# Performance work log

Hardware: AMD Instinct MI355X
Metric: run time of the kernel (lower is better)

The kernel has to match this reference:

```python
import jax, jax.numpy as jnp
import numpy as np
import math

N_HEADS = 4
N_ITERS = 2  # SSFormer n=2; each loop iteration recomputes the same values (no feedback in the original code)
BN_EPS = 1e-5


def _attention(q, k, v):
    """SSTransformer: multi-head cross-attention over flattened spatial dims.
    q,k,v: [B, C, H, W] -> returns [B, C, L] with L = H*W.
    """
    b, c = q.shape[0], q.shape[1]
    L = q.shape[2] * q.shape[3]
    ch = c // N_HEADS
    scale = 1.0 / math.sqrt(math.sqrt(ch))
    qf = (q.reshape(b * N_HEADS, ch, L) * scale)
    kf = (k.reshape(b * N_HEADS, ch, L) * scale)
    vf = v.reshape(b * N_HEADS, ch, L)
    # weight: [B*H, t, s]
    w = jnp.einsum('bct,bcs->bts', qf, kf)
    w = jax.nn.softmax(w.astype(jnp.float32), axis=-1).astype(w.dtype)
    a = jnp.einsum('bts,bcs->bct', w, vf)
    return a.reshape(b, c, L)


def setup_inputs() -> dict:
    key = jax.random.key(0)
    k1, k2, k3, k4 = jax.random.split(key, 4)
    B, C, H, W = 8, 512, 32, 32
    c = jax.random.normal(k1, (B, C, H, W), dtype=jnp.float32)
    e = jax.random.normal(k2, (B, C, H, W), dtype=jnp.float32)
    conv_w = jax.random.normal(k3, (C, C, 1, 1), dtype=jnp.float32) / math.sqrt(C)
    conv_b = jax.random.normal(k4, (C,), dtype=jnp.float32) * 0.02
    bn_gamma = jnp.ones((C,), dtype=jnp.float32)
    bn_beta = jnp.zeros((C,), dtype=jnp.float32)
    return {"c": c, "e": e, "conv_w": conv_w, "conv_b": conv_b,
            "bn_gamma": bn_gamma, "bn_beta": bn_beta}


def reference(c, e, conv_w, conv_b, bn_gamma, bn_beta):
    bs, ch, h, w = c.shape
    L = h * w
    for _ in range(N_ITERS):
        _c = _attention(e, c, c)                       # [B, C, L]
        _e = _attention(_c.reshape(bs, ch, h, w), e, e)  # [B, C, L]
    _e = _e.reshape(bs, ch, h, w)
    # Proj: 1x1 conv + BatchNorm2d (training-mode batch stats) + Swish
    x = jnp.einsum('oc,bchw->bohw', conv_w.reshape(ch, ch), _e) + conv_b[None, :, None, None]
    mean = jnp.mean(x, axis=(0, 2, 3), keepdims=True)
    var = jnp.var(x, axis=(0, 2, 3), keepdims=True)
    xn = (x - mean) * jax.lax.rsqrt(var + BN_EPS)
    xn = xn * bn_gamma[None, :, None, None] + bn_beta[None, :, None, None]
    return xn * jax.nn.sigmoid(xn)
```

## Files before the change

### kernel.cpp

```cpp
#include <hip/hip_runtime.h>
#include <hip/hip_bf16.h>

typedef __attribute__((ext_vector_type(8))) short short8;
typedef __attribute__((ext_vector_type(4))) float floatx4;
typedef __attribute__((ext_vector_type(4))) float f32x4;
typedef unsigned short u16;
typedef unsigned int u32;
typedef __attribute__((ext_vector_type(2))) unsigned int u32x2;
typedef __attribute__((ext_vector_type(4))) unsigned int u32x4;
typedef __attribute__((ext_vector_type(8))) unsigned short ushort8;

#define LSEQ 1024
#define CHD  128
#define CEXP 0.12751744900425577f
#define THR_RAW 62.73318f

static __device__ __forceinline__ u16 f2b(float f) {
  __hip_bfloat16 h = __float2bfloat16(f);
  return *reinterpret_cast<u16*>(&h);
}
static __device__ __forceinline__ u32 cvtpk(float a, float b) {
  u32 r;
  asm("v_cvt_pk_bf16_f32 %0, %1, %2" : "=v"(r) : "v"(a), "v"(b));
  return r;
}
static __device__ __forceinline__ float exp2f_fast(float x) {
  float r;
  asm("v_exp_f32 %0, %1" : "=v"(r) : "v"(x));
  return r;
}
static __device__ __forceinline__ void gl_lds16(const void* g, void* l) {
  __builtin_amdgcn_global_load_lds((__attribute__((address_space(1))) const void*)g,
                                   (__attribute__((address_space(3))) void*)l, 16, 0, 0);
}

__global__ __launch_bounds__(256) void k_prep(const float* __restrict__ cin,
                                              const float* __restrict__ ein,
                                              const float* __restrict__ Wf,
                                              u16* __restrict__ cV, u16* __restrict__ cT,
                                              u16* __restrict__ eV, u16* __restrict__ eT,
                                              u16* __restrict__ wb, float* __restrict__ zbuf) {
  __shared__ u16 tile[32][72];
  int z = blockIdx.z;
  int tid = threadIdx.x;
  if (z >= 64) {
    int wblk = (z - 64) * 64 + blockIdx.y * 16 + blockIdx.x;
    int base = (wblk * 256 + tid) * 8;
    f32x4 a = *(const f32x4*)(Wf + base);
    f32x4 b = *(const f32x4*)(Wf + base + 4);
    u32x4 u;
    u[0] = cvtpk(a[0], a[1]); u[1] = cvtpk(a[2], a[3]);
    u[2] = cvtpk(b[0], b[1]); u[3] = cvtpk(b[2], b[3]);
    *(u32x4*)(wb + base) = u;
    if (wblk == 0) {
      f32x4 zz; zz[0]=0.f; zz[1]=0.f; zz[2]=0.f; zz[3]=0.f;
      *(f32x4*)(zbuf + tid * 4) = zz;
    }
    return;
  }
  const float* in = (z < 32) ? cin : ein;
  u16* outV = (z < 32) ? cV : eV;
  u16* outT = (z < 32) ? cT : eT;
  int bh = z & 31, c0 = blockIdx.y * 32, s0 = blockIdx.x * 64;
  int cl = tid >> 3, sc = tid & 7;
  size_t off = ((size_t)bh * CHD + c0 + cl) * LSEQ + s0 + sc * 8;
  f32x4 a = *(const f32x4*)(in + off);
  f32x4 b = *(const f32x4*)(in + off + 4);
  u32x4 u;
  u[0] = cvtpk(a[0], a[1]); u[1] = cvtpk(a[2], a[3]);
  u[2] = cvtpk(b[0], b[1]); u[3] = cvtpk(b[2], b[3]);
  *(u32x4*)(outV + off) = u;
  *(u32x4*)&tile[cl][sc * 8] = u;
  __syncthreads();
  int sl = tid >> 2, cc = tid & 3;
  ushort8 v;
#pragma unroll
  for (int j = 0; j < 8; ++j) v[j] = tile[cc * 8 + j][sl];
  *(ushort8*)(outT + ((size_t)bh * LSEQ + s0 + sl) * CHD + c0 + cc * 8) = v;
}

__global__ __launch_bounds__(256) void k_attn(const u16* __restrict__ eT,
                                              const u16* __restrict__ cT,
                                              const u16* __restrict__ cV,
                                              const u16* __restrict__ eV,
                                              u16* __restrict__ outT) {
  __shared__ char ldsbuf[73728];

  int bh = blockIdx.x, tt = blockIdx.y;
  int tid = threadIdx.x;
  int w = tid >> 6, lane = tid & 63;
  int lo = lane & 15, hi = lane >> 4;
  int t0 = tt * 64 + w * 16;

  char* pw = ldsbuf + 65536 + w * 2048 + lo * 128;
  int sw = (lo & 7) << 4;

  auto stageK = [&](int buf, int sb, const char* kTb) {
    char* dst = ldsbuf + buf * 16384;
#pragma unroll
    for (int it = 0; it < 4; ++it) {
      int bb = it * 4096 + tid * 16;
      int row = bb >> 8;
      int cb = (bb & 255) ^ ((row & 7) << 4);
      gl_lds16(kTb + (size_t)(sb * 64 + row) * 256 + cb, dst + bb);
    }
  };
  auto stageV = [&](int buf, int sb, const char* vb) {
    char* dst = ldsbuf + 32768 + buf * 16384;
#pragma unroll
    for (int it = 0; it < 4; ++it) {
      int bb = it * 4096 + tid * 16;
      int row = bb >> 7;
      int cb = (bb & 127) ^ ((row & 7) << 4);
      gl_lds16(vb + (size_t)row * 2048 + sb * 128 + cb, dst + bb);
    }
  };

  short8 bq[4];
  floatx4 oacc[8];
  float m_r, l_r;

  auto flash = [&](const char* kTb, const char* vb) {
    m_r = -1e30f; l_r = 0.f;
#pragma unroll
    for (int i = 0; i < 8; ++i) { oacc[i][0]=0.f; oacc[i][1]=0.f; oacc[i][2]=0.f; oacc[i][3]=0.f; }
    stageK(0, 0, kTb); stageV(0, 0, vb);
    for (int sb = 0; sb < 16; ++sb) {
      int cur = sb & 1;
      __builtin_amdgcn_s_barrier();
      if (sb < 15) { stageK(cur ^ 1, sb + 1, kTb); stageV(cur ^ 1, sb + 1, vb); }
      if (sb < 15) { asm volatile("s_waitcnt vmcnt(8)" ::: "memory"); }
      else         { asm volatile("s_waitcnt vmcnt(0)" ::: "memory"); }
      __builtin_amdgcn_s_barrier();

      const char* ldsK = ldsbuf + cur * 16384;
      const char* ldsV = ldsbuf + 32768 + cur * 16384;

      float sa[4][4];
      __builtin_amdgcn_s_setprio(1);
#pragma unroll
      for (int ss = 0; ss < 4; ++ss) {
        floatx4 acc; acc[0]=0.f; acc[1]=0.f; acc[2]=0.f; acc[3]=0.f;
        int row = ss * 16 + lo;
#pragma unroll
        for (int ks = 0; ks < 4; ++ks) {
          int cbyte = (ks * 64 + hi * 16) ^ ((row & 7) << 4);
          short8 a = *(const short8*)(ldsK + row * 256 + cbyte);
          acc = __builtin_amdgcn_mfma_f32_16x16x32_bf16(a, bq[ks], acc, 0, 0, 0);
        }
#pragma unroll
        for (int r = 0; r < 4; ++r) sa[ss][r] = acc[r];
      }
      __builtin_amdgcn_s_setprio(0);

      float x0 = fmaxf(fmaxf(sa[0][0], sa[0][1]), sa[0][2]);
      float x1 = fmaxf(fmaxf(sa[0][3], sa[1][0]), sa[1][1]);
      float x2 = fmaxf(fmaxf(sa[1][2], sa[1][3]), sa[2][0]);
      float x3 = fmaxf(fmaxf(sa[2][1], sa[2][2]), sa[2][3]);
      float x4 = fmaxf(fmaxf(sa[3][0], sa[3][1]), sa[3][2]);
      float bm = fmaxf(fmaxf(fmaxf(x0, x1), fmaxf(x2, x3)), fmaxf(x4, sa[3][3]));
      bm = fmaxf(bm, __shfl_xor(bm, 16));
      bm = fmaxf(bm, __shfl_xor(bm, 32));

      bool stay = __all(bm - m_r <= THR_RAW);
      if (!stay) {
        float mn = fmaxf(m_r, bm);
        float corr = exp2f_fast((m_r - mn) * CEXP);
        m_r = mn;
        l_r *= corr;
#pragma unroll
        for (int i = 0; i < 8; ++i) {
          oacc[i][0] *= corr; oacc[i][1] *= corr; oacc[i][2] *= corr; oacc[i][3] *= corr;
        }
      }
      float mnC = m_r * CEXP;

      float rs = 0.f;
#pragma unroll
      for (int ss = 0; ss < 4; ++ss)
#pragma unroll
        for (int r = 0; r < 4; ++r) {
          float p = exp2f_fast(__builtin_fmaf(sa[ss][r], CEXP, -mnC));
          sa[ss][r] = p;
          rs += p;
        }
      rs += __shfl_xor(rs, 16);
      rs += __shfl_xor(rs, 32);
      l_r += rs;

#pragma unroll
      for (int ss = 0; ss < 4; ++ss) {
        u32x2 pk;
        pk[0] = cvtpk(sa[ss][0], sa[ss][1]);
        pk[1] = cvtpk(sa[ss][2], sa[ss][3]);
        *(u32x2*)(pw + ((ss * 32 + hi * 8) ^ sw)) = pk;
      }
      asm volatile("" ::: "memory");

      short8 bp0 = *(const short8*)(pw + ((hi * 16) ^ sw));
      short8 bp1 = *(const short8*)(pw + ((64 + hi * 16) ^ sw));
      __builtin_amdgcn_s_setprio(1);
#pragma unroll
      for (int mt = 0; mt < 8; ++mt) {
        int crow = mt * 16 + lo;
        const char* va = ldsV + crow * 128;
        int vsw = (crow & 7) << 4;
        short8 a0 = *(const short8*)(va + ((hi * 16) ^ vsw));
        short8 a1 = *(const short8*)(va + ((64 + hi * 16) ^ vsw));
        oacc[mt] = __builtin_amdgcn_mfma_f32_16x16x32_bf16(a0, bp0, oacc[mt], 0, 0, 0);
        oacc[mt] = __builtin_amdgcn_mfma_f32_16x16x32_bf16(a1, bp1, oacc[mt], 0, 0, 0);
      }
      __builtin_amdgcn_s_setprio(0);
    }
  };

  const u16* qbase = eT + ((size_t)bh * LSEQ + t0 + lo) * CHD + hi * 8;
#pragma unroll
  for (int ks = 0; ks < 4; ++ks) bq[ks] = *(const short8*)(qbase + ks * 32);

  flash((const char*)(cT + (size_t)bh * LSEQ * CHD),
        (const char*)(cV + (size_t)bh * CHD * LSEQ));

  {
    float inv = 1.0f / l_r;
    char* ot = ldsbuf + w * 4096;
#pragma unroll
    for (int mt = 0; mt < 8; ++mt) {
      u32x2 pk;
      pk[0] = cvtpk(oacc[mt][0] * inv, oacc[mt][1] * inv);
      pk[1] = cvtpk(oacc[mt][2] * inv, oacc[mt][3] * inv);
      *(u32x2*)(ot + lo * 256 + ((mt * 32 + hi * 8) ^ ((lo & 7) << 4))) = pk;
    }
    asm volatile("" ::: "memory");
#pragma unroll
    for (int ks = 0; ks < 4; ++ks) {
      int cb = (ks * 64 + hi * 16) ^ ((lo & 7) << 4);
      bq[ks] = *(const short8*)(ot + lo * 256 + cb);
    }
  }
  __syncthreads();

  flash((const char*)(eT + (size_t)bh * LSEQ * CHD),
        (const char*)(eV + (size_t)bh * CHD * LSEQ));

  float inv = 1.0f / l_r;
  char* ot = ldsbuf + w * 4096;
#pragma unroll
  for (int mt = 0; mt < 8; ++mt) {
    u32x2 pk;
    pk[0] = cvtpk(oacc[mt][0] * inv, oacc[mt][1] * inv);
    pk[1] = cvtpk(oacc[mt][2] * inv, oacc[mt][3] * inv);
    *(u32x2*)(ot + lo * 256 + ((mt * 32 + hi * 8) ^ ((lo & 7) << 4))) = pk;
  }
  asm volatile("" ::: "memory");
  u16* orow = outT + ((size_t)bh * LSEQ + t0 + lo) * CHD;
#pragma unroll
  for (int it = 0; it < 4; ++it) {
    int cb = (it * 64 + hi * 16) ^ ((lo & 7) << 4);
    ushort8 d = *(const ushort8*)(ot + lo * 256 + cb);
    *(ushort8*)(orow + it * 32 + hi * 8) = d;
  }
}

__global__ __launch_bounds__(256) void k_proj(const u16* __restrict__ Wm,
                                              const u16* __restrict__ eT,
                                              const float* __restrict__ bias,
                                              u16* __restrict__ x,
                                              float* __restrict__ chsum,
                                              float* __restrict__ chsq) {
  __shared__ char lds[65536];
  int lt = blockIdx.x, ot = blockIdx.y;
  int b = lt >> 3;
  int l0b = (lt & 7) * 128;
  int o0 = ot * 128;
  int tid = threadIdx.x, w = tid >> 6, lane = tid & 63, lo = lane & 15, hi = lane >> 4;
  int wm = w >> 1, wn = w & 1;
  const char* Wb = (const char*)Wm;
  const char* eTb = (const char*)eT;

  auto stageA = [&](int buf, int kb) {
    char* dst = lds + buf * 16384;
#pragma unroll
    for (int it = 0; it < 4; ++it) {
      int bb = it * 4096 + tid * 16;
      int row = bb >> 7;
      int cb = (bb & 127) ^ ((row & 7) << 4);
      gl_lds16(Wb + (size_t)(o0 + row) * 1024 + kb * 128 + cb, dst + bb);
    }
  };
  auto stageB = [&](int buf, int kb) {
    char* dst = lds + 32768 + buf * 16384;
    int page = b * 4 + (kb >> 1);
    int choff = (kb & 1) * 128;
#pragma unroll
    for (int it = 0; it < 4; ++it) {
      int bb = it * 4096 + tid * 16;
      int row = bb >> 7;
      int cb = (bb & 127) ^ ((row & 7) << 4);
      gl_lds16(eTb + ((size_t)page * 1024 + l0b + row) * 256 + choff + cb, dst + bb);
    }
  };

  floatx4 acc[4][4];
#pragma unroll
  for (int i = 0; i < 4; ++i)
#pragma unroll
    for (int j = 0; j < 4; ++j) { acc[i][j][0]=0.f; acc[i][j][1]=0.f; acc[i][j][2]=0.f; acc[i][j][3]=0.f; }

  stageA(0, 0); stageB(0, 0);

  for (int kb = 0; kb < 8; ++kb) {
    int cur = kb & 1;
    __builtin_amdgcn_s_barrier();
    if (kb < 7) { stageA(cur ^ 1, kb + 1); stageB(cur ^ 1, kb + 1); }
    if (kb < 7) { asm volatile("s_waitcnt vmcnt(8)" ::: "memory"); }
    else        { asm volatile("s_waitcnt vmcnt(0)" ::: "memory"); }
    __builtin_amdgcn_s_barrier();
    const char* A = lds + cur * 16384;
    const char* B = lds + 32768 + cur * 16384;
#pragma unroll
    for (int kk = 0; kk < 2; ++kk) {
      short8 af[4], bf[4];
#pragma unroll
      for (int mi = 0; mi < 4; ++mi) {
        int row = wm * 64 + mi * 16 + lo;
        af[mi] = *(const short8*)(A + row * 128 + ((kk * 64 + hi * 16) ^ ((row & 7) << 4)));
      }
#pragma unroll
      for (int ni = 0; ni < 4; ++ni) {
        int row = wn * 64 + ni * 16 + lo;
        bf[ni] = *(const short8*)(B + row * 128 + ((kk * 64 + hi * 16) ^ ((row & 7) << 4)));
      }
      __builtin_amdgcn_s_setprio(1);
#pragma unroll
      for (int mi = 0; mi < 4; ++mi)
#pragma unroll
        for (int ni = 0; ni < 4; ++ni)
          acc[mi][ni] = __builtin_amdgcn_mfma_f32_16x16x32_bf16(af[mi], bf[ni], acc[mi][ni], 0, 0, 0);
      __builtin_amdgcn_s_setprio(0);
    }
  }

#pragma unroll
  for (int mi = 0; mi < 4; ++mi) {
#pragma unroll
    for (int r = 0; r < 4; ++r) {
      int o = o0 + wm * 64 + mi * 16 + hi * 4 + r;
      float bv = bias[o];
      float s = 0.f, q = 0.f;
#pragma unroll
      for (int ni = 0; ni < 4; ++ni) {
        float xv = acc[mi][ni][r] + bv;
        x[((size_t)b * 512 + o) * LSEQ + l0b + wn * 64 + ni * 16 + lo] = f2b(xv);
        s += xv; q += xv * xv;
      }
#pragma unroll
      for (int d = 1; d < 16; d <<= 1) { s += __shfl_xor(s, d); q += __shfl_xor(q, d); }
      if (lo == 0) {
        atomicAdd(&chsum[o], s);
        atomicAdd(&chsq[o], q);
      }
    }
  }
}

__global__ __launch_bounds__(256) void k_final(const u16* __restrict__ x,
                                               const float* __restrict__ chsum,
                                               const float* __restrict__ chsq,
                                               const float* __restrict__ gamma,
                                               const float* __restrict__ beta,
                                               float* __restrict__ out) {
  int idx = blockIdx.x * 256 + threadIdx.x;
  int base = idx * 8;
  int ch = (base >> 10) & 511;
  const float invn = 1.0f / 8192.0f;
  float mean = chsum[ch] * invn;
  float var = chsq[ch] * invn - mean * mean;
  float rstd = rsqrtf(var + 1e-5f);
  float sc = gamma[ch] * rstd;
  float sh = beta[ch] - mean * sc;
  ushort8 vx = *(const ushort8*)(x + base);
  f32x4 o0, o1;
#pragma unroll
  for (int j = 0; j < 8; ++j) {
    union { u32 i; float f; } cv; cv.i = ((u32)vx[j]) << 16;
    float xn = cv.f * sc + sh;
    float sg = 1.0f / (1.0f + __expf(-xn));
    float r = xn * sg;
    if (j < 4) o0[j] = r; else o1[j - 4] = r;
  }
  *(f32x4*)(out + base) = o0;
  *(f32x4*)(out + base + 4) = o1;
}

extern "C" void kernel_launch(void* const* d_in, const int* in_sizes, int n_in,
                              void* d_out, int out_size, void* d_ws, size_t ws_size,
                              hipStream_t stream) {
  const float* c     = (const float*)d_in[0];
  const float* e     = (const float*)d_in[1];
  const float* Wf    = (const float*)d_in[2];
  const float* bias  = (const float*)d_in[3];
  const float* gamma = (const float*)d_in[4];
  const float* beta  = (const float*)d_in[5];
  float* outp = (float*)d_out;

  char* ws = (char*)d_ws;
  const size_t TB = (size_t)32 * 1024 * 128 * 2;
  u16* eT  = (u16*)(ws);
  u16* cT  = (u16*)(ws + TB);
  u16* cV  = (u16*)(ws + 2 * TB);
  u16* eV  = (u16*)(ws + 3 * TB);
  u16* xT  = (u16*)(ws + 4 * TB);
  u16* Wbf = (u16*)(ws + 5 * TB);
  float* chsum = (float*)(ws + 5 * TB + (1 << 20));
  float* chsq  = chsum + 512;
  u16* x   = (u16*)(ws + 6 * TB);

  dim3 tb(256);

  k_prep<<<dim3(16, 4, 66), tb, 0, stream>>>(c, e, Wf, cV, cT, eV, eT, Wbf, chsum);
  k_attn<<<dim3(32, 16), tb, 0, stream>>>(eT, cT, cV, eV, xT);
  k_proj<<<dim3(64, 4), tb, 0, stream>>>(Wbf, xT, bias, x, chsum, chsq);
  k_final<<<dim3(2048), tb, 0, stream>>>(x, chsum, chsq, gamma, beta, outp);
}
```

Baseline: 109.2 us.

## Split attention keys across two blocks and merge partial softmax outputs

Each fused two-stage attention block is replaced by two launches of a split-KV flash kernel. Every launch halves the key range per block, doubles the grid, and halves LDS so more blocks fit per CU. A separate merge kernel combines the two partial outputs using the saved max and sum values. This raises parallelism and occupancy at the cost of extra global writes and reads for the partial results and more kernel launches. Workspace buffers are reused for the intermediates.

Result: slower. 130.6 us (+19.6%).

```diff
diff --git a/kernel.cpp b/kernel.cpp
--- a/kernel.cpp
+++ b/kernel.cpp
@@ -4,6 +4,7 @@
 typedef __attribute__((ext_vector_type(8))) short short8;
 typedef __attribute__((ext_vector_type(4))) float floatx4;
 typedef __attribute__((ext_vector_type(4))) float f32x4;
+typedef __attribute__((ext_vector_type(2))) float f32x2;
 typedef unsigned short u16;
 typedef unsigned int u32;
 typedef __attribute__((ext_vector_type(2))) unsigned int u32x2;
@@ -15,9 +16,8 @@
 #define CEXP 0.12751744900425577f
 #define THR_RAW 62.73318f
 
-static __device__ __forceinline__ u16 f2b(float f) {
-  __hip_bfloat16 h = __float2bfloat16(f);
-  return *reinterpret_cast<u16*>(&h);
+static __device__ __forceinline__ float b2f(u16 u) {
+  union { u32 i; float f; } x; x.i = ((u32)u) << 16; return x.f;
 }
 static __device__ __forceinline__ u32 cvtpk(float a, float b) {
   u32 r;
@@ -79,187 +79,187 @@
   *(ushort8*)(outT + ((size_t)bh * LSEQ + s0 + sl) * CHD + c0 + cc * 8) = v;
 }
 
-__global__ __launch_bounds__(256) void k_attn(const u16* __restrict__ eT,
-                                              const u16* __restrict__ cT,
-                                              const u16* __restrict__ cV,
-                                              const u16* __restrict__ eV,
-                                              u16* __restrict__ outT) {
-  __shared__ char ldsbuf[73728];
-
-  int bh = blockIdx.x, tt = blockIdx.y;
+__global__ __launch_bounds__(256, 4) void k_attn(const u16* __restrict__ qT,
+                                                 const u16* __restrict__ kT,
+                                                 const u16* __restrict__ v,
+                                                 u16* __restrict__ O0,
+                                                 u16* __restrict__ O1,
+                                                 float* __restrict__ ml) {
+  __shared__ char ldsbuf[36864];
+
+  int bh = blockIdx.x, tt = blockIdx.y, sh = blockIdx.z;
   int tid = threadIdx.x;
   int w = tid >> 6, lane = tid & 63;
   int lo = lane & 15, hi = lane >> 4;
   int t0 = tt * 64 + w * 16;
 
-  char* pw = ldsbuf + 65536 + w * 2048 + lo * 128;
-  int sw = (lo & 7) << 4;
-
-  auto stageK = [&](int buf, int sb, const char* kTb) {
-    char* dst = ldsbuf + buf * 16384;
-#pragma unroll
-    for (int it = 0; it < 4; ++it) {
+  const char* kTb = (const char*)(kT + (size_t)bh * LSEQ * CHD) + (size_t)sh * 512 * 256;
+  const char* vb  = (const char*)(v  + (size_t)bh * CHD * LSEQ) + sh * 1024;
+
+  char* pw = ldsbuf + 32768 + w * 1024 + lo * 64;
+  int swp = (lo & 3) << 4;
+
+  auto stageK = [&](int buf, int sb) {
+    char* dst = ldsbuf + buf * 8192;
+#pragma unroll
+    for (int it = 0; it < 2; ++it) {
       int bb = it * 4096 + tid * 16;
       int row = bb >> 8;
       int cb = (bb & 255) ^ ((row & 7) << 4);
-      gl_lds16(kTb + (size_t)(sb * 64 + row) * 256 + cb, dst + bb);
+      gl_lds16(kTb + (size_t)(sb * 32 + row) * 256 + cb, dst + bb);
     }
   };
-  auto stageV = [&](int buf, int sb, const char* vb) {
-    char* dst = ldsbuf + 32768 + buf * 16384;
-#pragma unroll
-    for (int it = 0; it < 4; ++it) {
+  auto stageV = [&](int buf, int sb) {
+    char* dst = ldsbuf + 16384 + buf * 8192;
+#pragma unroll
+    for (int it = 0; it < 2; ++it) {
       int bb = it * 4096 + tid * 16;
-      int row = bb >> 7;
-      int cb = (bb & 127) ^ ((row & 7) << 4);
-      gl_lds16(vb + (size_t)row * 2048 + sb * 128 + cb, dst + bb);
+      int row = bb >> 6;
+      int cb = (bb & 63) ^ ((row & 3) << 4);
+      gl_lds16(vb + (size_t)row * 2048 + sb * 64 + cb, dst + bb);
     }
   };
 
+  const u16* qbase = qT + ((size_t)bh * LSEQ + t0 + lo) * CHD + hi * 8;
   short8 bq[4];
+#pragma unroll
+  for (int ks = 0; ks < 4; ++ks) bq[ks] = *(const short8*)(qbase + ks * 32);
+
   floatx4 oacc[8];
-  float m_r, l_r;
-
-  auto flash = [&](const char* kTb, const char* vb) {
-    m_r = -1e30f; l_r = 0.f;
-#pragma unroll
-    for (int i = 0; i < 8; ++i) { oacc[i][0]=0.f; oacc[i][1]=0.f; oacc[i][2]=0.f; oacc[i][3]=0.f; }
-    stageK(0, 0, kTb); stageV(0, 0, vb);
-    for (int sb = 0; sb < 16; ++sb) {
-      int cur = sb & 1;
-      __builtin_amdgcn_s_barrier();
-      if (sb < 15) { stageK(cur ^ 1, sb + 1, kTb); stageV(cur ^ 1, sb + 1, vb); }
-      if (sb < 15) { asm volatile("s_waitcnt vmcnt(8)" ::: "memory"); }
-      else         { asm volatile("s_waitcnt vmcnt(0)" ::: "memory"); }
-      __builtin_amdgcn_s_barrier();
-
-      const char* ldsK = ldsbuf + cur * 16384;
-      const char* ldsV = ldsbuf + 32768 + cur * 16384;
-
-      float sa[4][4];
-      __builtin_amdgcn_s_setprio(1);
-#pragma unroll
-      for (int ss = 0; ss < 4; ++ss) {
-        floatx4 acc; acc[0]=0.f; acc[1]=0.f; acc[2]=0.f; acc[3]=0.f;
-        int row = ss * 16 + lo;
-#pragma unroll
-        for (int ks = 0; ks < 4; ++ks) {
-          int cbyte = (ks * 64 + hi * 16) ^ ((row & 7) << 4);
-          short8 a = *(const short8*)(ldsK + row * 256 + cbyte);
-          acc = __builtin_amdgcn_mfma_f32_16x16x32_bf16(a, bq[ks], acc, 0, 0, 0);
-        }
-#pragma unroll
-        for (int r = 0; r < 4; ++r) sa[ss][r] = acc[r];
-      }
-      __builtin_amdgcn_s_setprio(0);
-
-      float x0 = fmaxf(fmaxf(sa[0][0], sa[0][1]), sa[0][2]);
-      float x1 = fmaxf(fmaxf(sa[0][3], sa[1][0]), sa[1][1]);
-      float x2 = fmaxf(fmaxf(sa[1][2], sa[1][3]), sa[2][0]);
-      float x3 = fmaxf(fmaxf(sa[2][1], sa[2][2]), sa[2][3]);
-      float x4 = fmaxf(fmaxf(sa[3][0], sa[3][1]), sa[3][2]);
-      float bm = fmaxf(fmaxf(fmaxf(x0, x1), fmaxf(x2, x3)), fmaxf(x4, sa[3][3]));
-      bm = fmaxf(bm, __shfl_xor(bm, 16));
-      bm = fmaxf(bm, __shfl_xor(bm, 32));
-
-      bool stay = __all(bm - m_r <= THR_RAW);
-      if (!stay) {
-        float mn = fmaxf(m_r, bm);
-        float corr = exp2f_fast((m_r - mn) * CEXP);
-        m_r = mn;
-        l_r *= corr;
-#pragma unroll
-        for (int i = 0; i < 8; ++i) {
-          oacc[i][0] *= corr; oacc[i][1] *= corr; oacc[i][2] *= corr; oacc[i][3] *= corr;
-        }
-      }
-      float mnC = m_r * CEXP;
-
-      float rs = 0.f;
-#pragma unroll
-      for (int ss = 0; ss < 4; ++ss)
-#pragma unroll
-        for (int r = 0; r < 4; ++r) {
-          float p = exp2f_fast(__builtin_fmaf(sa[ss][r], CEXP, -mnC));
-          sa[ss][r] = p;
-          rs += p;
-        }
-      rs += __shfl_xor(rs, 16);
-      rs += __shfl_xor(rs, 32);
-      l_r += rs;
-
-#pragma unroll
-      for (int ss = 0; ss < 4; ++ss) {
-        u32x2 pk;
-        pk[0] = cvtpk(sa[ss][0], sa[ss][1]);
-        pk[1] = cvtpk(sa[ss][2], sa[ss][3]);
-        *(u32x2*)(pw + ((ss * 32 + hi * 8) ^ sw)) = pk;
-      }
-      asm volatile("" ::: "memory");
-
-      short8 bp0 = *(const short8*)(pw + ((hi * 16) ^ sw));
-      short8 bp1 = *(const short8*)(pw + ((64 + hi * 16) ^ sw));
-      __builtin_amdgcn_s_setprio(1);
-#pragma unroll
-      for (int mt = 0; mt < 8; ++mt) {
-        int crow = mt * 16 + lo;
-        const char* va = ldsV + crow * 128;
-        int vsw = (crow & 7) << 4;
-        short8 a0 = *(const short8*)(va + ((hi * 16) ^ vsw));
-        short8 a1 = *(const short8*)(va + ((64 + hi * 16) ^ vsw));
-        oacc[mt] = __builtin_amdgcn_mfma_f32_16x16x32_bf16(a0, bp0, oacc[mt], 0, 0, 0);
-        oacc[mt] = __builtin_amdgcn_mfma_f32_16x16x32_bf16(a1, bp1, oacc[mt], 0, 0, 0);
-      }
-      __builtin_amdgcn_s_setprio(0);
-    }
-  };
-
-  const u16* qbase = eT + ((size_t)bh * LSEQ + t0 + lo) * CHD + hi * 8;
-#pragma unroll
-  for (int ks = 0; ks < 4; ++ks) bq[ks] = *(const short8*)(qbase + ks * 32);
-
-  flash((const char*)(cT + (size_t)bh * LSEQ * CHD),
-        (const char*)(cV + (size_t)bh * CHD * LSEQ));
-
-  {
-    float inv = 1.0f / l_r;
-    char* ot = ldsbuf + w * 4096;
+#pragma unroll
+  for (int i = 0; i < 8; ++i) { oacc[i][0]=0.f; oacc[i][1]=0.f; oacc[i][2]=0.f; oacc[i][3]=0.f; }
+  float m_r = -1e30f, l_r = 0.f;
+
+  stageK(0, 0); stageV(0, 0);
+  for (int sb = 0; sb < 16; ++sb) {
+    int cur = sb & 1;
+    __builtin_amdgcn_s_barrier();
+    if (sb < 15) { stageK(cur ^ 1, sb + 1); stageV(cur ^ 1, sb + 1); }
+    if (sb < 15) { asm volatile("s_waitcnt vmcnt(4)" ::: "memory"); }
+    else         { asm volatile("s_waitcnt vmcnt(0)" ::: "memory"); }
+    __builtin_amdgcn_s_barrier();
+
+    const char* ldsK = ldsbuf + cur * 8192;
+    const char* ldsV = ldsbuf + 16384 + cur * 8192;
+
+    float sa[2][4];
+    __builtin_amdgcn_s_setprio(1);
+#pragma unroll
+    for (int ss = 0; ss < 2; ++ss) {
+      floatx4 acc; acc[0]=0.f; acc[1]=0.f; acc[2]=0.f; acc[3]=0.f;
+      int row = ss * 16 + lo;
+#pragma unroll
+      for (int ks = 0; ks < 4; ++ks) {
+        int cbyte = (ks * 64 + hi * 16) ^ ((row & 7) << 4);
+        short8 a = *(const short8*)(ldsK + row * 256 + cbyte);
+        acc = __builtin_amdgcn_mfma_f32_16x16x32_bf16(a, bq[ks], acc, 0, 0, 0);
+      }
+#pragma unroll
+      for (int r = 0; r < 4; ++r) sa[ss][r] = acc[r];
+    }
+    __builtin_amdgcn_s_setprio(0);
+
+    float x0 = fmaxf(fmaxf(sa[0][0], sa[0][1]), sa[0][2]);
+    float x1 = fmaxf(fmaxf(sa[0][3], sa[1][0]), sa[1][1]);
+    float bm = fmaxf(fmaxf(x0, x1), fmaxf(sa[1][2], sa[1][3]));
+    bm = fmaxf(bm, __shfl_xor(bm, 16));
+    bm = fmaxf(bm, __shfl_xor(bm, 32));
+
+    bool stay = __all(bm - m_r <= THR_RAW);
+    if (!stay) {
+      float mn = fmaxf(m_r, bm);
+      float corr = exp2f_fast((m_r - mn) * CEXP);
+      m_r = mn;
+      l_r *= corr;
+#pragma unroll
+      for (int i = 0; i < 8; ++i) {
+        oacc[i][0] *= corr; oacc[i][1] *= corr; oacc[i][2] *= corr; oacc[i][3] *= corr;
+      }
+    }
+    float mnC = m_r * CEXP;
+
+    float rs = 0.f;
+#pragma unroll
+    for (int ss = 0; ss < 2; ++ss)
+#pragma unroll
+      for (int r = 0; r < 4; ++r) {
+        float p = exp2f_fast(__builtin_fmaf(sa[ss][r], CEXP, -mnC));
+        sa[ss][r] = p;
+        rs += p;
+      }
+    rs += __shfl_xor(rs, 16);
+    rs += __shfl_xor(rs, 32);
+    l_r += rs;
+
+#pragma unroll
+    for (int ss = 0; ss < 2; ++ss) {
+      u32x2 pk;
+      pk[0] = cvtpk(sa[ss][0], sa[ss][1]);
+      pk[1] = cvtpk(sa[ss][2], sa[ss][3]);
+      *(u32x2*)(pw + ((ss * 32 + hi * 8) ^ swp)) = pk;
+    }
+    asm volatile("" ::: "memory");
+
+    short8 bp = *(const short8*)(pw + ((hi * 16) ^ swp));
+    __builtin_amdgcn_s_setprio(1);
 #pragma unroll
     for (int mt = 0; mt < 8; ++mt) {
-      u32x2 pk;
-      pk[0] = cvtpk(oacc[mt][0] * inv, oacc[mt][1] * inv);
-      pk[1] = cvtpk(oacc[mt][2] * inv, oacc[mt][3] * inv);
-      *(u32x2*)(ot + lo * 256 + ((mt * 32 + hi * 8) ^ ((lo & 7) << 4))) = pk;
-    }
-    asm volatile("" ::: "memory");
-#pragma unroll
-    for (int ks = 0; ks < 4; ++ks) {
-      int cb = (ks * 64 + hi * 16) ^ ((lo & 7) << 4);
-      bq[ks] = *(const short8*)(ot + lo * 256 + cb);
-    }
-  }
+      int crow = mt * 16 + lo;
+      short8 a = *(const short8*)(ldsV + crow * 64 + ((hi * 16) ^ ((crow & 3) << 4)));
+      oacc[mt] = __builtin_amdgcn_mfma_f32_16x16x32_bf16(a, bp, oacc[mt], 0, 0, 0);
+    }
+    __builtin_amdgcn_s_setprio(0);
+  }
+
   __syncthreads();
 
-  flash((const char*)(eT + (size_t)bh * LSEQ * CHD),
-        (const char*)(eV + (size_t)bh * CHD * LSEQ));
-
-  float inv = 1.0f / l_r;
   char* ot = ldsbuf + w * 4096;
 #pragma unroll
   for (int mt = 0; mt < 8; ++mt) {
     u32x2 pk;
-    pk[0] = cvtpk(oacc[mt][0] * inv, oacc[mt][1] * inv);
-    pk[1] = cvtpk(oacc[mt][2] * inv, oacc[mt][3] * inv);
+    pk[0] = cvtpk(oacc[mt][0], oacc[mt][1]);
+    pk[1] = cvtpk(oacc[mt][2], oacc[mt][3]);
     *(u32x2*)(ot + lo * 256 + ((mt * 32 + hi * 8) ^ ((lo & 7) << 4))) = pk;
   }
   asm volatile("" ::: "memory");
-  u16* orow = outT + ((size_t)bh * LSEQ + t0 + lo) * CHD;
+  u16* obase = (sh ? O1 : O0) + ((size_t)bh * LSEQ + t0 + lo) * CHD;
 #pragma unroll
   for (int it = 0; it < 4; ++it) {
     int cb = (it * 64 + hi * 16) ^ ((lo & 7) << 4);
     ushort8 d = *(const ushort8*)(ot + lo * 256 + cb);
-    *(ushort8*)(orow + it * 32 + hi * 8) = d;
-  }
+    *(ushort8*)(obase + it * 32 + hi * 8) = d;
+  }
+  if (hi == 0) {
+    f32x2 p; p[0] = m_r; p[1] = l_r;
+    *(f32x2*)(ml + ((size_t)sh * 32768 + bh * LSEQ + t0 + lo) * 2) = p;
+  }
+}
+
+__global__ __launch_bounds__(256) void k_merge(const u16* __restrict__ O0,
+                                               const u16* __restrict__ O1,
+                                               const float* __restrict__ ml,
+                                               u16* __restrict__ outT) {
+  int idx = blockIdx.x * 256 + threadIdx.x;
+  int tg = idx >> 4;
+  int cs = idx & 15;
+  f32x2 ml0 = *(const f32x2*)(ml + (size_t)tg * 2);
+  f32x2 ml1 = *(const f32x2*)(ml + (size_t)(32768 + tg) * 2);
+  float m = fmaxf(ml0[0], ml1[0]);
+  float e0 = exp2f_fast((ml0[0] - m) * CEXP);
+  float e1 = exp2f_fast((ml1[0] - m) * CEXP);
+  float inv = 1.0f / (ml0[1] * e0 + ml1[1] * e1);
+  float s0 = e0 * inv, s1 = e1 * inv;
+  size_t off = (size_t)tg * 128 + cs * 8;
+  ushort8 a = *(const ushort8*)(O0 + off);
+  ushort8 b = *(const ushort8*)(O1 + off);
+  u32x4 o;
+#pragma unroll
+  for (int j = 0; j < 4; ++j) {
+    float f0 = b2f(a[2 * j]) * s0 + b2f(b[2 * j]) * s1;
+    float f1 = b2f(a[2 * j + 1]) * s0 + b2f(b[2 * j + 1]) * s1;
+    o[j] = cvtpk(f0, f1);
+  }
+  *(u32x4*)(outT + off) = o;
 }
 
 __global__ __launch_bounds__(256) void k_proj(const u16* __restrict__ Wm,
@@ -351,7 +351,7 @@
 #pragma unroll
       for (int ni = 0; ni < 4; ++ni) {
         float xv = acc[mi][ni][r] + bv;
-        x[((size_t)b * 512 + o) * LSEQ + l0b + wn * 64 + ni * 16 + lo] = f2b(xv);
+        x[((size_t)b * 512 + o) * LSEQ + l0b + wn * 64 + ni * 16 + lo] = cvtpk(xv, xv) & 0xffff;
         s += xv; q += xv * xv;
       }
 #pragma unroll
@@ -383,8 +383,7 @@
   f32x4 o0, o1;
 #pragma unroll
   for (int j = 0; j < 8; ++j) {
-    union { u32 i; float f; } cv; cv.i = ((u32)vx[j]) << 16;
-    float xn = cv.f * sc + sh;
+    float xn = b2f(vx[j]) * sc + sh;
     float sg = 1.0f / (1.0f + __expf(-xn));
     float r = xn * sg;
     if (j < 4) o0[j] = r; else o1[j - 4] = r;
@@ -410,16 +409,22 @@
   u16* cT  = (u16*)(ws + TB);
   u16* cV  = (u16*)(ws + 2 * TB);
   u16* eV  = (u16*)(ws + 3 * TB);
-  u16* xT  = (u16*)(ws + 4 * TB);
-  u16* Wbf = (u16*)(ws + 5 * TB);
-  float* chsum = (float*)(ws + 5 * TB + (1 << 20));
+  u16* cT2 = (u16*)(ws + 4 * TB);
+  u16* xT  = (u16*)(ws + 5 * TB);
+  u16* pB  = (u16*)(ws + 6 * TB);
+  u16* Wbf = (u16*)(ws + 7 * TB);
+  float* chsum = (float*)(ws + 7 * TB + (1 << 20));
   float* chsq  = chsum + 512;
-  u16* x   = (u16*)(ws + 6 * TB);
+  float* ml    = (float*)(ws + 7 * TB + (1 << 20) + 8192);
+  u16* x = pB;
 
   dim3 tb(256);
 
   k_prep<<<dim3(16, 4, 66), tb, 0, stream>>>(c, e, Wf, cV, cT, eV, eT, Wbf, chsum);
-  k_attn<<<dim3(32, 16), tb, 0, stream>>>(eT, cT, cV, eV, xT);
+  k_attn<<<dim3(32, 16, 2), tb, 0, stream>>>(eT, cT, cV, xT, pB, ml);
+  k_merge<<<dim3(2048), tb, 0, stream>>>(xT, pB, ml, cT2);
+  k_attn<<<dim3(32, 16, 2), tb, 0, stream>>>(cT2, eT, eV, cT, cV, ml);
+  k_merge<<<dim3(2048), tb, 0, stream>>>(cT, cV, ml, xT);
   k_proj<<<dim3(64, 4), tb, 0, stream>>>(Wbf, xT, bias, x, chsum, chsq);
   k_final<<<dim3(2048), tb, 0, stream>>>(x, chsum, chsq, gamma, beta, outp);
 }
```

## Switch attention to 32x32x16 MFMA with register-level P transpose via permlane32 swap

Applied to the files above, without the earlier changes.

Rewrites the fused two-pass flash attention kernel to use 32x32x16 bf16 MFMA tiles, with two waves per block, each handling 32 query rows. The probability matrix and the intermediate attention output are repacked into MFMA B operands in registers using v_permlane32_swap instead of going through LDS, which removes LDS round trips and a block barrier. The aim is fewer MFMA instructions, fewer LDS reads and fewer reductions per key block, at the cost of higher register pressure and half the threads per block staging loads.

After: 112.8 us. 3.2% more time.

```diff
diff --git a/kernel.cpp b/kernel.cpp
--- a/kernel.cpp
+++ b/kernel.cpp
@@ -4,6 +4,7 @@
 typedef __attribute__((ext_vector_type(8))) short short8;
 typedef __attribute__((ext_vector_type(4))) float floatx4;
 typedef __attribute__((ext_vector_type(4))) float f32x4;
+typedef __attribute__((ext_vector_type(16))) float f32x16;
 typedef unsigned short u16;
 typedef unsigned int u32;
 typedef __attribute__((ext_vector_type(2))) unsigned int u32x2;
@@ -15,6 +16,9 @@
 #define CEXP 0.12751744900425577f
 #define THR_RAW 62.73318f
 
+static __device__ __forceinline__ float b2f(u16 u) {
+  union { u32 i; float f; } x; x.i = ((u32)u) << 16; return x.f;
+}
 static __device__ __forceinline__ u16 f2b(float f) {
   __hip_bfloat16 h = __float2bfloat16(f);
   return *reinterpret_cast<u16*>(&h);
@@ -23,6 +27,14 @@
   u32 r;
   asm("v_cvt_pk_bf16_f32 %0, %1, %2" : "=v"(r) : "v"(a), "v"(b));
   return r;
+}
+static __device__ __forceinline__ void swap32(u32& a, u32& b) {
+  asm("v_permlane32_swap_b32 %0, %1" : "+v"(a), "+v"(b));
+}
+static __device__ __forceinline__ short8 mk8(u32 a, u32 b, u32 c, u32 d) {
+  union { u32x4 u; short8 s; } x;
+  x.u[0] = a; x.u[1] = b; x.u[2] = c; x.u[3] = d;
+  return x.s;
 }
 static __device__ __forceinline__ float exp2f_fast(float x) {
   float r;
@@ -79,186 +91,190 @@
   *(ushort8*)(outT + ((size_t)bh * LSEQ + s0 + sl) * CHD + c0 + cc * 8) = v;
 }
 
-__global__ __launch_bounds__(256) void k_attn(const u16* __restrict__ eT,
+__global__ __launch_bounds__(128) void k_attn(const u16* __restrict__ eT,
                                               const u16* __restrict__ cT,
                                               const u16* __restrict__ cV,
                                               const u16* __restrict__ eV,
                                               u16* __restrict__ outT) {
-  __shared__ char ldsbuf[73728];
-
-  int bh = blockIdx.x, tt = blockIdx.y;
+  __shared__ char ldsbuf[65536];
+
+  int tt = blockIdx.x, bh = blockIdx.y;
   int tid = threadIdx.x;
   int w = tid >> 6, lane = tid & 63;
-  int lo = lane & 15, hi = lane >> 4;
-  int t0 = tt * 64 + w * 16;
-
-  char* pw = ldsbuf + 65536 + w * 2048 + lo * 128;
-  int sw = (lo & 7) << 4;
+  int ln = lane & 31, h = lane >> 5;
+  int t0 = tt * 64 + w * 32;
 
   auto stageK = [&](int buf, int sb, const char* kTb) {
     char* dst = ldsbuf + buf * 16384;
 #pragma unroll
-    for (int it = 0; it < 4; ++it) {
-      int bb = it * 4096 + tid * 16;
+    for (int it = 0; it < 8; ++it) {
+      int bb = it * 2048 + tid * 16;
       int row = bb >> 8;
-      int cb = (bb & 255) ^ ((row & 7) << 4);
+      int cb = (bb & 255) ^ ((row & 15) << 4);
       gl_lds16(kTb + (size_t)(sb * 64 + row) * 256 + cb, dst + bb);
     }
   };
   auto stageV = [&](int buf, int sb, const char* vb) {
     char* dst = ldsbuf + 32768 + buf * 16384;
 #pragma unroll
-    for (int it = 0; it < 4; ++it) {
-      int bb = it * 4096 + tid * 16;
+    for (int it = 0; it < 8; ++it) {
+      int bb = it * 2048 + tid * 16;
       int row = bb >> 7;
       int cb = (bb & 127) ^ ((row & 7) << 4);
       gl_lds16(vb + (size_t)row * 2048 + sb * 128 + cb, dst + bb);
     }
   };
 
-  short8 bq[4];
-  floatx4 oacc[8];
+  short8 bq[8];
+  f32x16 oacc[4];
   float m_r, l_r;
 
   auto flash = [&](const char* kTb, const char* vb) {
     m_r = -1e30f; l_r = 0.f;
 #pragma unroll
-    for (int i = 0; i < 8; ++i) { oacc[i][0]=0.f; oacc[i][1]=0.f; oacc[i][2]=0.f; oacc[i][3]=0.f; }
+    for (int i = 0; i < 4; ++i)
+#pragma unroll
+      for (int r = 0; r < 16; ++r) oacc[i][r] = 0.f;
+
     stageK(0, 0, kTb); stageV(0, 0, vb);
     for (int sb = 0; sb < 16; ++sb) {
       int cur = sb & 1;
       __builtin_amdgcn_s_barrier();
       if (sb < 15) { stageK(cur ^ 1, sb + 1, kTb); stageV(cur ^ 1, sb + 1, vb); }
-      if (sb < 15) { asm volatile("s_waitcnt vmcnt(8)" ::: "memory"); }
+      if (sb < 15) { asm volatile("s_waitcnt vmcnt(16)" ::: "memory"); }
       else         { asm volatile("s_waitcnt vmcnt(0)" ::: "memory"); }
       __builtin_amdgcn_s_barrier();
 
       const char* ldsK = ldsbuf + cur * 16384;
       const char* ldsV = ldsbuf + 32768 + cur * 16384;
 
-      float sa[4][4];
+      f32x16 sa0, sa1;
+#pragma unroll
+      for (int r = 0; r < 16; ++r) { sa0[r] = 0.f; sa1[r] = 0.f; }
       __builtin_amdgcn_s_setprio(1);
 #pragma unroll
-      for (int ss = 0; ss < 4; ++ss) {
-        floatx4 acc; acc[0]=0.f; acc[1]=0.f; acc[2]=0.f; acc[3]=0.f;
-        int row = ss * 16 + lo;
-#pragma unroll
-        for (int ks = 0; ks < 4; ++ks) {
-          int cbyte = (ks * 64 + hi * 16) ^ ((row & 7) << 4);
-          short8 a = *(const short8*)(ldsK + row * 256 + cbyte);
-          acc = __builtin_amdgcn_mfma_f32_16x16x32_bf16(a, bq[ks], acc, 0, 0, 0);
-        }
-#pragma unroll
-        for (int r = 0; r < 4; ++r) sa[ss][r] = acc[r];
+      for (int k = 0; k < 8; ++k) {
+        int col = k * 32 + (h << 4);
+        int r0 = ln, r1 = 32 + ln;
+        short8 a0 = *(const short8*)(ldsK + r0 * 256 + (col ^ ((r0 & 15) << 4)));
+        short8 a1 = *(const short8*)(ldsK + r1 * 256 + (col ^ ((r1 & 15) << 4)));
+        sa0 = __builtin_amdgcn_mfma_f32_32x32x16_bf16(a0, bq[k], sa0, 0, 0, 0);
+        sa1 = __builtin_amdgcn_mfma_f32_32x32x16_bf16(a1, bq[k], sa1, 0, 0, 0);
       }
       __builtin_amdgcn_s_setprio(0);
 
-      float x0 = fmaxf(fmaxf(sa[0][0], sa[0][1]), sa[0][2]);
-      float x1 = fmaxf(fmaxf(sa[0][3], sa[1][0]), sa[1][1]);
-      float x2 = fmaxf(fmaxf(sa[1][2], sa[1][3]), sa[2][0]);
-      float x3 = fmaxf(fmaxf(sa[2][1], sa[2][2]), sa[2][3]);
-      float x4 = fmaxf(fmaxf(sa[3][0], sa[3][1]), sa[3][2]);
-      float bm = fmaxf(fmaxf(fmaxf(x0, x1), fmaxf(x2, x3)), fmaxf(x4, sa[3][3]));
-      bm = fmaxf(bm, __shfl_xor(bm, 16));
+      float bm = sa0[0];
+#pragma unroll
+      for (int r = 1; r < 16; ++r) bm = fmaxf(bm, sa0[r]);
+#pragma unroll
+      for (int r = 0; r < 16; ++r) bm = fmaxf(bm, sa1[r]);
       bm = fmaxf(bm, __shfl_xor(bm, 32));
 
       bool stay = __all(bm - m_r <= THR_RAW);
       if (!stay) {
         float mn = fmaxf(m_r, bm);
         float corr = exp2f_fast((m_r - mn) * CEXP);
-        m_r = mn;
-        l_r *= corr;
-#pragma unroll
-        for (int i = 0; i < 8; ++i) {
-          oacc[i][0] *= corr; oacc[i][1] *= corr; oacc[i][2] *= corr; oacc[i][3] *= corr;
-        }
+        m_r = mn; l_r *= corr;
+#pragma unroll
+        for (int i = 0; i < 4; ++i)
+#pragma unroll
+          for (int r = 0; r < 16; ++r) oacc[i][r] *= corr;
       }
       float mnC = m_r * CEXP;
 
       float rs = 0.f;
 #pragma unroll
-      for (int ss = 0; ss < 4; ++ss)
-#pragma unroll
-        for (int r = 0; r < 4; ++r) {
-          float p = exp2f_fast(__builtin_fmaf(sa[ss][r], CEXP, -mnC));
-          sa[ss][r] = p;
-          rs += p;
-        }
-      rs += __shfl_xor(rs, 16);
+      for (int r = 0; r < 16; ++r) {
+        float p = exp2f_fast(__builtin_fmaf(sa0[r], CEXP, -mnC));
+        sa0[r] = p; rs += p;
+      }
+#pragma unroll
+      for (int r = 0; r < 16; ++r) {
+        float p = exp2f_fast(__builtin_fmaf(sa1[r], CEXP, -mnC));
+        sa1[r] = p; rs += p;
+      }
       rs += __shfl_xor(rs, 32);
       l_r += rs;
 
-#pragma unroll
-      for (int ss = 0; ss < 4; ++ss) {
-        u32x2 pk;
-        pk[0] = cvtpk(sa[ss][0], sa[ss][1]);
-        pk[1] = cvtpk(sa[ss][2], sa[ss][3]);
-        *(u32x2*)(pw + ((ss * 32 + hi * 8) ^ sw)) = pk;
-      }
-      asm volatile("" ::: "memory");
-
-      short8 bp0 = *(const short8*)(pw + ((hi * 16) ^ sw));
-      short8 bp1 = *(const short8*)(pw + ((64 + hi * 16) ^ sw));
+      short8 bp[4];
+      {
+        u32 w0 = cvtpk(sa0[0], sa0[1]),  w1 = cvtpk(sa0[2], sa0[3]);
+        u32 w2 = cvtpk(sa0[4], sa0[5]),  w3 = cvtpk(sa0[6], sa0[7]);
+        swap32(w0, w2); swap32(w1, w3);
+        bp[0] = mk8(w0, w1, w2, w3);
+        u32 w4 = cvtpk(sa0[8], sa0[9]),  w5 = cvtpk(sa0[10], sa0[11]);
+        u32 w6 = cvtpk(sa0[12], sa0[13]), w7 = cvtpk(sa0[14], sa0[15]);
+        swap32(w4, w6); swap32(w5, w7);
+        bp[1] = mk8(w4, w5, w6, w7);
+        u32 x0 = cvtpk(sa1[0], sa1[1]),  x1 = cvtpk(sa1[2], sa1[3]);
+        u32 x2 = cvtpk(sa1[4], sa1[5]),  x3 = cvtpk(sa1[6], sa1[7]);
+        swap32(x0, x2); swap32(x1, x3);
+        bp[2] = mk8(x0, x1, x2, x3);
+        u32 x4 = cvtpk(sa1[8], sa1[9]),  x5 = cvtpk(sa1[10], sa1[11]);
+        u32 x6 = cvtpk(sa1[12], sa1[13]), x7 = cvtpk(sa1[14], sa1[15]);
+        swap32(x4, x6); swap32(x5, x7);
+        bp[3] = mk8(x4, x5, x6, x7);
+      }
+
       __builtin_amdgcn_s_setprio(1);
 #pragma unroll
-      for (int mt = 0; mt < 8; ++mt) {
-        int crow = mt * 16 + lo;
-        const char* va = ldsV + crow * 128;
-        int vsw = (crow & 7) << 4;
-        short8 a0 = *(const short8*)(va + ((hi * 16) ^ vsw));
-        short8 a1 = *(const short8*)(va + ((64 + hi * 16) ^ vsw));
-        oacc[mt] = __builtin_amdgcn_mfma_f32_16x16x32_bf16(a0, bp0, oacc[mt], 0, 0, 0);
-        oacc[mt] = __builtin_amdgcn_mfma_f32_16x16x32_bf16(a1, bp1, oacc[mt], 0, 0, 0);
+      for (int ks = 0; ks < 4; ++ks) {
+        int col = ks * 32 + (h << 4);
+#pragma unroll
+        for (int m = 0; m < 4; ++m) {
+          int row = m * 32 + ln;
+          short8 a = *(const short8*)(ldsV + row * 128 + (col ^ ((row & 7) << 4)));
+          oacc[m] = __builtin_amdgcn_mfma_f32_32x32x16_bf16(a, bp[ks], oacc[m], 0, 0, 0);
+        }
       }
       __builtin_amdgcn_s_setprio(0);
     }
   };
 
-  const u16* qbase = eT + ((size_t)bh * LSEQ + t0 + lo) * CHD + hi * 8;
-#pragma unroll
-  for (int ks = 0; ks < 4; ++ks) bq[ks] = *(const short8*)(qbase + ks * 32);
+  const u16* qbase = eT + ((size_t)bh * LSEQ + t0 + ln) * CHD + h * 8;
+#pragma unroll
+  for (int k = 0; k < 8; ++k) bq[k] = *(const short8*)(qbase + k * 16);
 
   flash((const char*)(cT + (size_t)bh * LSEQ * CHD),
         (const char*)(cV + (size_t)bh * CHD * LSEQ));
 
   {
     float inv = 1.0f / l_r;
-    char* ot = ldsbuf + w * 4096;
-#pragma unroll
-    for (int mt = 0; mt < 8; ++mt) {
-      u32x2 pk;
-      pk[0] = cvtpk(oacc[mt][0] * inv, oacc[mt][1] * inv);
-      pk[1] = cvtpk(oacc[mt][2] * inv, oacc[mt][3] * inv);
-      *(u32x2*)(ot + lo * 256 + ((mt * 32 + hi * 8) ^ ((lo & 7) << 4))) = pk;
-    }
-    asm volatile("" ::: "memory");
-#pragma unroll
-    for (int ks = 0; ks < 4; ++ks) {
-      int cb = (ks * 64 + hi * 16) ^ ((lo & 7) << 4);
-      bq[ks] = *(const short8*)(ot + lo * 256 + cb);
-    }
-  }
-  __syncthreads();
+#pragma unroll
+    for (int m = 0; m < 4; ++m) {
+      u32 w0 = cvtpk(oacc[m][0]*inv,  oacc[m][1]*inv),  w1 = cvtpk(oacc[m][2]*inv,  oacc[m][3]*inv);
+      u32 w2 = cvtpk(oacc[m][4]*inv,  oacc[m][5]*inv),  w3 = cvtpk(oacc[m][6]*inv,  oacc[m][7]*inv);
+      swap32(w0, w2); swap32(w1, w3);
+      bq[2*m] = mk8(w0, w1, w2, w3);
+      u32 w4 = cvtpk(oacc[m][8]*inv,  oacc[m][9]*inv),  w5 = cvtpk(oacc[m][10]*inv, oacc[m][11]*inv);
+      u32 w6 = cvtpk(oacc[m][12]*inv, oacc[m][13]*inv), w7 = cvtpk(oacc[m][14]*inv, oacc[m][15]*inv);
+      swap32(w4, w6); swap32(w5, w7);
+      bq[2*m+1] = mk8(w4, w5, w6, w7);
+    }
+  }
 
   flash((const char*)(eT + (size_t)bh * LSEQ * CHD),
         (const char*)(eV + (size_t)bh * CHD * LSEQ));
 
-  float inv = 1.0f / l_r;
-  char* ot = ldsbuf + w * 4096;
-#pragma unroll
-  for (int mt = 0; mt < 8; ++mt) {
-    u32x2 pk;
-    pk[0] = cvtpk(oacc[mt][0] * inv, oacc[mt][1] * inv);
-    pk[1] = cvtpk(oacc[mt][2] * inv, oacc[mt][3] * inv);
-    *(u32x2*)(ot + lo * 256 + ((mt * 32 + hi * 8) ^ ((lo & 7) << 4))) = pk;
-  }
-  asm volatile("" ::: "memory");
-  u16* orow = outT + ((size_t)bh * LSEQ + t0 + lo) * CHD;
-#pragma unroll
-  for (int it = 0; it < 4; ++it) {
-    int cb = (it * 64 + hi * 16) ^ ((lo & 7) << 4);
-    ushort8 d = *(const ushort8*)(ot + lo * 256 + cb);
-    *(ushort8*)(orow + it * 32 + hi * 8) = d;
+  {
+    float inv = 1.0f / l_r;
+    char* ot = ldsbuf + w * 8192;
+#pragma unroll
+    for (int m = 0; m < 4; ++m)
+#pragma unroll
+      for (int q = 0; q < 8; ++q) {
+        u32 pk = cvtpk(oacc[m][2*q] * inv, oacc[m][2*q+1] * inv);
+        int c2 = m * 64 + 4 * (q & 1) + 16 * (q >> 1) + 8 * h;
+        *(u32*)(ot + ln * 256 + (c2 ^ ((ln & 7) << 4))) = pk;
+      }
+    asm volatile("" ::: "memory");
+    u16* orow = outT + ((size_t)bh * LSEQ + t0 + ln) * CHD;
+#pragma unroll
+    for (int it = 0; it < 8; ++it) {
+      int col = h * 128 + it * 16;
+      ushort8 d = *(const ushort8*)(ot + ln * 256 + (col ^ ((ln & 7) << 4)));
+      *(ushort8*)((char*)orow + col) = d;
+    }
   }
 }
 
@@ -383,8 +399,7 @@
   f32x4 o0, o1;
 #pragma unroll
   for (int j = 0; j < 8; ++j) {
-    union { u32 i; float f; } cv; cv.i = ((u32)vx[j]) << 16;
-    float xn = cv.f * sc + sh;
+    float xn = b2f(vx[j]) * sc + sh;
     float sg = 1.0f / (1.0f + __expf(-xn));
     float r = xn * sg;
     if (j < 4) o0[j] = r; else o1[j - 4] = r;
@@ -419,7 +434,7 @@
   dim3 tb(256);
 
   k_prep<<<dim3(16, 4, 66), tb, 0, stream>>>(c, e, Wf, cV, cT, eV, eT, Wbf, chsum);
-  k_attn<<<dim3(32, 16), tb, 0, stream>>>(eT, cT, cV, eV, xT);
+  k_attn<<<dim3(16, 32), dim3(128), 0, stream>>>(eT, cT, cV, eV, xT);
   k_proj<<<dim3(64, 4), tb, 0, stream>>>(Wbf, xT, bias, x, chsum, chsq);
   k_final<<<dim3(2048), tb, 0, stream>>>(x, chsum, chsq, gamma, beta, outp);
 }
```
